# Kernel optimization log

Hardware: AMD Instinct MI355X
Metric: run time of the kernel (lower is better)

## Reference

```python
import jax, jax.numpy as jnp
import numpy as np

GROUPS = 32
EPS = 1e-5

def setup_inputs() -> dict:
    key = jax.random.key(0)
    k1, k2, k3 = jax.random.split(key, 3)
    C = 512
    x = jax.random.normal(k1, (4, C, 64, 64), dtype=jnp.float32)
    gn_weight = jnp.ones((C,), jnp.float32)
    gn_bias = jnp.zeros((C,), jnp.float32)
    qkv_weight = jax.random.normal(k2, (3 * C, C), jnp.float32) * (1.0 / np.sqrt(C))
    proj_weight = jax.random.normal(k3, (C, C), jnp.float32) * (1.0 / np.sqrt(C))
    proj_bias = jnp.zeros((C,), jnp.float32)
    return {"x": x, "gn_weight": gn_weight, "gn_bias": gn_bias,
            "qkv_weight": qkv_weight, "proj_weight": proj_weight, "proj_bias": proj_bias}

def reference(x, gn_weight, gn_bias, qkv_weight, proj_weight, proj_bias):
    n, c, h, w = x.shape
    residue = x
    # GroupNorm(32, c): normalize over (c//32 channels * h * w) per group
    xg = x.reshape(n, GROUPS, -1)
    mu = xg.mean(axis=-1, keepdims=True)
    var = xg.var(axis=-1, keepdims=True)
    xn = (xg - mu) * jax.lax.rsqrt(var + EPS)
    xn = xn.reshape(n, c, h, w) * gn_weight[None, :, None, None] + gn_bias[None, :, None, None]
    # tokens: [n, T, c] with T = h*w
    t = xn.reshape(n, c, h * w).transpose(0, 2, 1)
    # qkv linear (no bias), n_heads = 1 so head_size = c
    qkv = jnp.einsum('ntc,dc->ntd', t, qkv_weight)
    q, k, v = jnp.split(qkv, 3, axis=-1)
    scale = 1.0 / np.sqrt(c)
    scores = jnp.einsum('nqc,nkc->nqk', q, k) * scale  # [n, T, T]
    weights = jax.nn.softmax(scores, axis=-1)
    out = jnp.einsum('nqk,nkc->nqc', weights, v)
    out = jnp.einsum('ntc,dc->ntd', out, proj_weight) + proj_bias
    out = out.transpose(0, 2, 1).reshape(n, c, h, w)
    return out + residue
```

## Files before the change

### kernel.cpp

```cpp
#include <hip/hip_runtime.h>
#include <hip/hip_bf16.h>

typedef __bf16 bf16;
typedef __bf16 bf16x4 __attribute__((ext_vector_type(4)));
typedef __bf16 bf16x8 __attribute__((ext_vector_type(8)));
typedef float f32x4 __attribute__((ext_vector_type(4)));

__device__ __forceinline__ void gload_lds16(const bf16* g, bf16* l) {
    __builtin_amdgcn_global_load_lds(
        (const __attribute__((address_space(1))) void*)g,
        (__attribute__((address_space(3))) void*)l, 16, 0, 0);
}

__global__ __launch_bounds__(256) void k_pre(const float* __restrict__ x,
                                             const float* __restrict__ qw,
                                             const float* __restrict__ pw,
                                             float2* __restrict__ part,
                                             bf16* __restrict__ qwb,
                                             bf16* __restrict__ pwb) {
    const int b = blockIdx.x;
    if (b < 1024) {
        const float4* p = (const float4*)(x + (long)b * 8192);
        float s = 0.f, ss = 0.f;
        #pragma unroll
        for (int i = 0; i < 8; ++i) {
            float4 v = p[threadIdx.x + i * 256];
            s  += v.x + v.y + v.z + v.w;
            ss += v.x * v.x + v.y * v.y + v.z * v.z + v.w * v.w;
        }
        #pragma unroll
        for (int off = 32; off >= 1; off >>= 1) {
            s  += __shfl_down(s, off);
            ss += __shfl_down(ss, off);
        }
        __shared__ float rs[4], rss[4];
        if ((threadIdx.x & 63) == 0) { rs[threadIdx.x >> 6] = s; rss[threadIdx.x >> 6] = ss; }
        __syncthreads();
        if (threadIdx.x == 0)
            part[b] = make_float2(rs[0] + rs[1] + rs[2] + rs[3],
                                  rss[0] + rss[1] + rss[2] + rss[3]);
    } else {
        const int i = (b - 1024) * 256 + threadIdx.x;
        if (i < 786432) {
            float v = qw[i];
            if (i < 512 * 512) v *= 0.06376281516217733f;
            qwb[i] = (bf16)v;
        } else {
            const int j = i - 786432;
            pwb[j] = (bf16)pw[j];
        }
    }
}

__global__ __launch_bounds__(256) void k_norm_t(const float* __restrict__ x,
                                                const float* __restrict__ w,
                                                const float* __restrict__ b,
                                                const float2* __restrict__ part,
                                                bf16* __restrict__ t) {
    __shared__ float tile[64][65];
    __shared__ float2 sgs[4];
    const int bid = blockIdx.x;
    const int n = bid >> 9, rem = bid & 511;
    const int s0 = (rem >> 3) * 64, c0 = (rem & 7) * 64;
    const int tid = threadIdx.x;
    const int sl = tid & 63, cq = tid >> 6;
    if (tid < 4) {
        const float2* pp = part + ((long)(n * 32 + (c0 >> 4) + tid)) * 8;
        float S = 0.f, SS = 0.f;
        #pragma unroll
        for (int j = 0; j < 8; ++j) { S += pp[j].x; SS += pp[j].y; }
        const float mu = S * (1.f / 65536.f);
        const float var = SS * (1.f / 65536.f) - mu * mu;
        sgs[tid] = make_float2(mu, rsqrtf(var + 1e-5f));
    }
    __syncthreads();
    #pragma unroll
    for (int i = 0; i < 16; ++i) {
        const int cl = cq * 16 + i;
        const int c = c0 + cl;
        const float2 st = sgs[cl >> 4];
        const float v = x[((long)(n * 512 + c)) * 4096 + s0 + sl];
        tile[cl][sl] = (v - st.x) * st.y * w[c] + b[c];
    }
    __syncthreads();
    #pragma unroll
    for (int i = 0; i < 16; ++i) {
        const int sl2 = cq * 16 + i;
        const int cl2 = tid & 63;
        t[((long)(n * 4096 + s0 + sl2)) * 512 + c0 + cl2] = (bf16)tile[cl2][sl2];
    }
}

#define PH(mh, kk, S_, WN)                                                         \
  {                                                                                \
    if ((mh) == 0) {                                                               \
      _Pragma("unroll")                                                            \
      for (int n = 0; n < 4; ++n) {                                                \
        int row = wn * 64 + n * 16 + lr;                                           \
        int cg = lg ^ ((row >> 1) & 3);                                            \
        bfr[n] = *(const bf16x8*)(BsT + (kk) * 8192 + row * 32 + cg * 8);          \
      }                                                                            \
    }                                                                              \
    _Pragma("unroll")                                                              \
    for (int i = 0; i < 4; ++i) {                                                  \
      int row = wm * 128 + ((mh) * 4 + i) * 16 + lr;                               \
      int cg = lg ^ ((row >> 1) & 3);                                              \
      af[i] = *(const bf16x8*)(AsT + (kk) * 8192 + row * 32 + cg * 8);             \
    }                                                                              \
    if ((S_) >= 0) issue_unit(S_);                                                 \
    __builtin_amdgcn_s_barrier();                                                  \
    asm volatile("" ::: "memory");                                                 \
    __builtin_amdgcn_s_setprio(1);                                                 \
    _Pragma("unroll")                                                              \
    for (int i = 0; i < 4; ++i)                                                    \
      _Pragma("unroll")                                                            \
      for (int n = 0; n < 4; ++n)                                                  \
        acc[(mh) * 4 + i][n] =                                                     \
            __builtin_amdgcn_mfma_f32_16x16x32_bf16(af[i], bfr[n],                 \
                                                    acc[(mh) * 4 + i][n], 0, 0, 0);\
    __builtin_amdgcn_s_setprio(0);                                                 \
    if constexpr ((WN) >= 0)                                                       \
      asm volatile("s_waitcnt vmcnt(%0)" ::"i"(WN) : "memory");                    \
    __builtin_amdgcn_s_barrier();                                                  \
    asm volatile("" ::: "memory");                                                 \
  }

template <int EPI>
__global__ __launch_bounds__(512, 2) void gemm256(
    const bf16* __restrict__ A, int lda, long aZ,
    const bf16* __restrict__ B, int ldb, long bZ,
    bf16* __restrict__ C, int ldc, long cZ, int K,
    bf16* __restrict__ Vt) {
    __shared__ bf16 As[2 * 2 * 256 * 32];
    __shared__ bf16 Bs[2 * 2 * 256 * 32];
    const int t = threadIdx.x;
    const int wid = t >> 6, l = t & 63;
    const int wm = wid >> 2, wn = wid & 3;
    const int lr = l & 15;
    const int lg = l >> 4;
    const long z = blockIdx.z;

    const int gx = gridDim.x;
    int nwg = gx * gridDim.y;
    int flat = blockIdx.y * gx + blockIdx.x;
    if ((nwg & 7) == 0) { int qq = nwg >> 3; flat = (flat & 7) * qq + (flat >> 3); }
    const int bx = flat % gx, by = flat / gx;

    const bf16* Ab = A + z * aZ + (long)bx * 256 * lda;
    const bf16* Bb = B + z * bZ + (long)by * 256 * ldb;

    const int NT = K >> 6;
    const int NT4 = NT << 2;

    f32x4 acc[8][4];
    #pragma unroll
    for (int i = 0; i < 8; ++i)
        #pragma unroll
        for (int n = 0; n < 4; ++n) acc[i][n] = f32x4{0.f, 0.f, 0.f, 0.f};

    const int srow = t >> 2;
    const int scg0 = t & 3;

    auto issue_unit = [&](int s) {
        int ti = s >> 2, idx = s & 3;
        int kh = idx >> 1, isB = idx & 1;
        const bf16* g = isB ? Bb : Ab;
        int ld = isB ? ldb : lda;
        bf16* lp = (isB ? Bs : As) + ((ti & 1) * 2 + kh) * 8192;
        int k0 = ti * 64 + kh * 32;
        #pragma unroll
        for (int j = 0; j < 2; ++j) {
            int row = j * 128 + srow;
            int cg = scg0 ^ ((row >> 1) & 3);
            gload_lds16(g + (long)row * ld + k0 + cg * 8, lp + (j * 512 + t) * 8);
        }
    };

    #pragma unroll
    for (int s = 0; s < 6; ++s) issue_unit(s);
    asm volatile("s_waitcnt vmcnt(8)" ::: "memory");
    __builtin_amdgcn_s_barrier();
    asm volatile("" ::: "memory");

    bf16x8 bfr[4], af[4];

    for (int ti = 0; ti < NT - 2; ++ti) {
        const bf16* AsT = As + (ti & 1) * 16384;
        const bf16* BsT = Bs + (ti & 1) * 16384;
        const int sb = 4 * ti + 6;
        PH(0, 0, sb + 0, -1)
        PH(1, 0, sb + 1, 8)
        PH(0, 1, sb + 2, -1)
        PH(1, 1, sb + 3, 8)
    }
    {
        const bf16* AsT = As + ((NT - 2) & 1) * 16384;
        const bf16* BsT = Bs + ((NT - 2) & 1) * 16384;
        PH(0, 0, NT4 - 2, -1)
        PH(1, 0, NT4 - 1, 8)
        PH(0, 1, -1, -1)
        PH(1, 1, -1, 4)
    }
    {
        const bf16* AsT = As + ((NT - 1) & 1) * 16384;
        const bf16* BsT = Bs + ((NT - 1) & 1) * 16384;
        PH(0, 0, -1, -1)
        PH(1, 0, -1, 0)
        PH(0, 1, -1, -1)
        PH(1, 1, -1, -1)
    }

    const int row0 = bx * 256 + wm * 128;
    const int col0 = by * 256 + wn * 64;
    const int rq = lg * 4;

    if (EPI == 1) {
        bf16* Cz = C + z * cZ;
        #pragma unroll
        for (int i = 0; i < 8; ++i)
            #pragma unroll
            for (int n = 0; n < 4; ++n) {
                const int col = col0 + n * 16 + lr;
                #pragma unroll
                for (int r = 0; r < 4; ++r)
                    Cz[(long)(row0 + i * 16 + rq + r) * ldc + col] = (bf16)exp2f(acc[i][n][r]);
            }
    } else {
        if (by < 4) {
            #pragma unroll
            for (int i = 0; i < 8; ++i) {
                const int row = row0 + i * 16 + rq;
                #pragma unroll
                for (int n = 0; n < 4; ++n) {
                    const int col = col0 + n * 16 + lr;
                    #pragma unroll
                    for (int r = 0; r < 4; ++r)
                        C[(long)(row + r) * 1024 + col] = (bf16)acc[i][n][r];
                }
            }
        } else {
            const int d0 = by * 256 - 1024;
            const int rb0 = bx * 256;
            const int nb = rb0 >> 12;
            const int sp0 = rb0 & 4095;
            bf16* Lt = As;
            #pragma unroll 1
            for (int q = 0; q < 4; ++q) {
                if (wn == q) {
                    #pragma unroll
                    for (int n = 0; n < 4; ++n) {
                        const int dl = n * 16 + lr;
                        const int a = dl & 7;
                        #pragma unroll
                        for (int i = 0; i < 8; ++i) {
                            const int sp = wm * 128 + i * 16 + rq;
                            const int g = sp >> 3;
                            bf16x4 v;
                            v[0] = (bf16)acc[i][n][0]; v[1] = (bf16)acc[i][n][1];
                            v[2] = (bf16)acc[i][n][2]; v[3] = (bf16)acc[i][n][3];
                            *(bf16x4*)(Lt + dl * 264 + ((g ^ a) * 8) + (sp & 7)) = v;
                        }
                    }
                }
                __syncthreads();
                {
                    const int dl = t >> 3, c8 = t & 7, a2 = dl & 7;
                    bf16* vd = Vt + ((long)nb * 512 + d0 + q * 64 + dl) * 4096 + sp0;
                    #pragma unroll
                    for (int j = 0; j < 4; ++j) {
                        const int gr = c8 + j * 8;
                        bf16x8 vv = *(const bf16x8*)(Lt + dl * 264 + ((gr ^ a2) * 8));
                        *(bf16x8*)(vd + gr * 8) = vv;
                    }
                }
                __syncthreads();
            }
        }
    }
}

__global__ __launch_bounds__(512, 1) void k_pv(
    const bf16* __restrict__ P, const bf16* __restrict__ Vt,
    bf16* __restrict__ O, int ldo) {
    __shared__ bf16 Bs[2][512 * 64];
    __shared__ bf16 As[2][64 * 64];
    __shared__ float linv[64];
    const int t = threadIdx.x;
    const int w = t >> 6, l = t & 63, lr = l & 15, lg = l >> 4;
    const int lr7 = lr & 7;
    const int sr = t >> 3, sc8 = t & 7, sr7 = sr & 7;
    const long zz = blockIdx.y;
    const int bx = blockIdx.x;

    const bf16* Pg = P + zz * ((long)4096 * 4096) + (long)(bx * 64 + sr) * 4096 + (sc8 ^ sr7) * 8;
    const bf16* Vg = Vt + zz * ((long)512 * 4096) + (long)sr * 4096 + (sc8 ^ sr7) * 8;

    auto issue = [&](int tile, int buf) {
        gload_lds16(Pg + tile * 64, As[buf] + t * 8);
        #pragma unroll
        for (int u = 0; u < 8; ++u)
            gload_lds16(Vg + (long)u * 64 * 4096 + tile * 64, Bs[buf] + u * 4096 + t * 8);
    };

    f32x4 acc[4][4];
    #pragma unroll
    for (int i = 0; i < 4; ++i)
        #pragma unroll
        for (int n = 0; n < 4; ++n) acc[i][n] = f32x4{0.f, 0.f, 0.f, 0.f};

    float lsum = 0.f;

    issue(0, 0);
    issue(1, 1);

    for (int ti = 0; ti < 64; ++ti) {
        if (ti < 63) { asm volatile("s_waitcnt vmcnt(9)" ::: "memory"); }
        else         { asm volatile("s_waitcnt vmcnt(0)" ::: "memory"); }
        __builtin_amdgcn_s_barrier();
        asm volatile("" ::: "memory");

        const bf16* Asb = As[ti & 1];
        const bf16* Bsb = Bs[ti & 1];

        {
            bf16x8 sv = *(const bf16x8*)(Asb + t * 8);
            #pragma unroll
            for (int j = 0; j < 8; ++j) lsum += (float)sv[j];
        }

        __builtin_amdgcn_s_setprio(1);
        #pragma unroll
        for (int kk = 0; kk < 2; ++kk) {
            bf16x8 af[4], bfv[4];
            #pragma unroll
            for (int mi = 0; mi < 4; ++mi)
                af[mi] = *(const bf16x8*)(Asb + (mi * 16 + lr) * 64 + (((kk * 4 + lg) ^ lr7) * 8));
            #pragma unroll
            for (int n = 0; n < 4; ++n)
                bfv[n] = *(const bf16x8*)(Bsb + (w * 64 + n * 16 + lr) * 64 + (((kk * 4 + lg) ^ lr7) * 8));
            #pragma unroll
            for (int mi = 0; mi < 4; ++mi)
                #pragma unroll
                for (int n = 0; n < 4; ++n)
                    acc[mi][n] = __builtin_amdgcn_mfma_f32_16x16x32_bf16(af[mi], bfv[n], acc[mi][n], 0, 0, 0);
        }
        __builtin_amdgcn_s_setprio(0);

        __builtin_amdgcn_s_barrier();
        asm volatile("" ::: "memory");
        if (ti < 62) issue(ti + 2, ti & 1);
    }

    lsum += __shfl_xor(lsum, 1);
    lsum += __shfl_xor(lsum, 2);
    lsum += __shfl_xor(lsum, 4);
    if (sc8 == 0) linv[sr] = 1.f / lsum;
    asm volatile("s_waitcnt lgkmcnt(0)" ::: "memory");
    __builtin_amdgcn_s_barrier();
    asm volatile("" ::: "memory");

    bf16* Oz = O + zz * ((long)4096 * ldo);
    #pragma unroll
    for (int mi = 0; mi < 4; ++mi) {
        float4 lv = *(const float4*)&linv[mi * 16 + lg * 4];
        #pragma unroll
        for (int n = 0; n < 4; ++n) {
            const long base = (long)(bx * 64 + mi * 16 + lg * 4) * ldo + w * 64 + n * 16 + lr;
            Oz[base]           = (bf16)(acc[mi][n][0] * lv.x);
            Oz[base + ldo]     = (bf16)(acc[mi][n][1] * lv.y);
            Oz[base + 2 * ldo] = (bf16)(acc[mi][n][2] * lv.z);
            Oz[base + 3 * ldo] = (bf16)(acc[mi][n][3] * lv.w);
        }
    }
}

#define PH128(nh, kk, S_, WN)                                                      \
  {                                                                                \
    if ((nh) == 0) {                                                               \
      _Pragma("unroll")                                                            \
      for (int i = 0; i < 4; ++i) {                                                \
        int row = wm * 64 + i * 16 + lr;                                           \
        int cg = lg ^ ((row >> 1) & 3);                                            \
        af[i] = *(const bf16x8*)(AsT + (kk) * 8192 + row * 32 + cg * 8);           \
      }                                                                            \
    }                                                                              \
    _Pragma("unroll")                                                              \
    for (int j = 0; j < 2; ++j) {                                                  \
      int row = wn * 64 + ((nh) * 2 + j) * 16 + lr;                                \
      int cg = lg ^ ((row >> 1) & 3);                                              \
      bfr[j] = *(const bf16x8*)(BsT + (kk) * 4096 + row * 32 + cg * 8);            \
    }                                                                              \
    if ((S_) >= 0) issue_unit(S_);                                                 \
    __builtin_amdgcn_s_barrier();                                                  \
    asm volatile("" ::: "memory");                                                 \
    __builtin_amdgcn_s_setprio(1);                                                 \
    _Pragma("unroll")                                                              \
    for (int i = 0; i < 4; ++i)                                                    \
      _Pragma("unroll")                                                            \
      for (int j = 0; j < 2; ++j)                                                  \
        acc[i][(nh) * 2 + j] =                                                     \
            __builtin_amdgcn_mfma_f32_16x16x32_bf16(af[i], bfr[j],                 \
                                                    acc[i][(nh) * 2 + j], 0, 0, 0);\
    __builtin_amdgcn_s_setprio(0);                                                 \
    if constexpr ((WN) >= 0)                                                       \
      asm volatile("s_waitcnt vmcnt(%0)" ::"i"(WN) : "memory");                    \
    __builtin_amdgcn_s_barrier();                                                  \
    asm volatile("" ::: "memory");                                                 \
  }

__global__ __launch_bounds__(512, 2) void gemm_proj(
    const bf16* __restrict__ A, int lda,
    const bf16* __restrict__ B, int ldb,
    const float* __restrict__ bias,
    const float* __restrict__ xres,
    float* __restrict__ outp) {
    __shared__ bf16 As[2 * 2 * 256 * 32];
    __shared__ bf16 Bs[2 * 2 * 128 * 32];
    const int t = threadIdx.x;
    const int wid = t >> 6, l = t & 63;
    const int wm = wid >> 1, wn = wid & 1;
    const int lr = l & 15;
    const int lg = l >> 4;

    const int gx = gridDim.x;
    int nwg = gx * gridDim.y;
    int flat = blockIdx.y * gx + blockIdx.x;
    if ((nwg & 7) == 0) { int qq = nwg >> 3; flat = (flat & 7) * qq + (flat >> 3); }
    const int bx = flat % gx, by = flat / gx;

    const bf16* Ab = A + (long)bx * 256 * lda;
    const bf16* Bb = B + (long)by * 128 * ldb;

    const int NT = 8;
    const int NT4 = 32;

    f32x4 acc[4][4];
    #pragma unroll
    for (int i = 0; i < 4; ++i)
        #pragma unroll
        for (int n = 0; n < 4; ++n) acc[i][n] = f32x4{0.f, 0.f, 0.f, 0.f};

    const int srow = t >> 2;
    const int scg0 = t & 3;

    auto issue_unit = [&](int s) {
        int ti = s >> 2, idx = s & 3;
        int kh = idx >> 1, isB = idx & 1;
        int k0 = ti * 64 + kh * 32;
        if (isB) {
            bf16* lp = Bs + ((ti & 1) * 2 + kh) * 4096;
            int cg = scg0 ^ ((srow >> 1) & 3);
            gload_lds16(Bb + (long)srow * ldb + k0 + cg * 8, lp + t * 8);
        } else {
            bf16* lp = As + ((ti & 1) * 2 + kh) * 8192;
            #pragma unroll
            for (int j = 0; j < 2; ++j) {
                int row = j * 128 + srow;
                int cg = scg0 ^ ((row >> 1) & 3);
                gload_lds16(Ab + (long)row * lda + k0 + cg * 8, lp + (j * 512 + t) * 8);
            }
        }
    };

    #pragma unroll
    for (int s = 0; s < 6; ++s) issue_unit(s);
    asm volatile("s_waitcnt vmcnt(6)" ::: "memory");
    __builtin_amdgcn_s_barrier();
    asm volatile("" ::: "memory");

    bf16x8 bfr[2], af[4];

    for (int ti = 0; ti < NT - 2; ++ti) {
        const bf16* AsT = As + (ti & 1) * 16384;
        const bf16* BsT = Bs + (ti & 1) * 8192;
        const int sb = 4 * ti + 6;
        PH128(0, 0, sb + 0, -1)
        PH128(1, 0, sb + 1, 6)
        PH128(0, 1, sb + 2, -1)
        PH128(1, 1, sb + 3, 6)
    }
    {
        const bf16* AsT = As + ((NT - 2) & 1) * 16384;
        const bf16* BsT = Bs + ((NT - 2) & 1) * 8192;
        PH128(0, 0, NT4 - 2, -1)
        PH128(1, 0, NT4 - 1, 6)
        PH128(0, 1, -1, -1)
        PH128(1, 1, -1, 3)
    }
    {
        const bf16* AsT = As + ((NT - 1) & 1) * 16384;
        const bf16* BsT = Bs + ((NT - 1) & 1) * 8192;
        PH128(0, 0, -1, -1)
        PH128(1, 0, -1, 0)
        PH128(0, 1, -1, -1)
        PH128(1, 1, -1, -1)
    }

    const int r0 = bx * 256;
    const int c0b = by * 128;
    const int nb = r0 >> 12;
    const int sp0 = r0 & 4095;
    const int rq = lg * 4;
    float* Lt = (float*)As;
    #pragma unroll
    for (int q = 0; q < 4; ++q) {
        if (wn == (q >> 1)) {
            #pragma unroll
            for (int nn = 0; nn < 2; ++nn) {
                const int n = (q & 1) * 2 + nn;
                const int cl = nn * 16 + lr;
                #pragma unroll
                for (int i = 0; i < 4; ++i) {
                    const int sp = wm * 64 + i * 16 + rq;
                    float4 v;
                    v.x = acc[i][n][0]; v.y = acc[i][n][1];
                    v.z = acc[i][n][2]; v.w = acc[i][n][3];
                    *(float4*)(Lt + cl * 260 + sp) = v;
                }
            }
        }
        __syncthreads();
        {
            const int cl2 = t >> 4;
            const int spc = (t & 15) * 16;
            const int col = c0b + q * 32 + cl2;
            const float bb = bias[col];
            const long ob = ((long)nb * 512 + col) * 4096 + sp0 + spc;
            #pragma unroll
            for (int j = 0; j < 4; ++j) {
                float4 lv = *(const float4*)(Lt + cl2 * 260 + spc + j * 4);
                float4 xv = *(const float4*)(xres + ob + j * 4);
                float4 ov;
                ov.x = lv.x + bb + xv.x; ov.y = lv.y + bb + xv.y;
                ov.z = lv.z + bb + xv.z; ov.w = lv.w + bb + xv.w;
                *(float4*)(outp + ob + j * 4) = ov;
            }
        }
        __syncthreads();
    }
}

extern "C" void kernel_launch(void* const* d_in, const int* in_sizes, int n_in,
                              void* d_out, int out_size, void* d_ws, size_t ws_size,
                              hipStream_t stream) {
    const float* x     = (const float*)d_in[0];
    const float* gnw   = (const float*)d_in[1];
    const float* gnb   = (const float*)d_in[2];
    const float* qkvw  = (const float*)d_in[3];
    const float* projw = (const float*)d_in[4];
    const float* projb = (const float*)d_in[5];

    char* ws = (char*)d_ws;
    size_t off = 0;
    auto alloc = [&](size_t bytes) {
        void* p = ws + off;
        off += (bytes + 255) & ~(size_t)255;
        return p;
    };
    bf16*   qwb   = (bf16*)alloc((size_t)1536 * 512 * 2);
    bf16*   pwb   = (bf16*)alloc((size_t)512 * 512 * 2);
    float2* part  = (float2*)alloc((size_t)1024 * 8);
    bf16*   qk    = (bf16*)alloc((size_t)16384 * 1024 * 2);
    bf16*   Vt    = (bf16*)alloc((size_t)4 * 512 * 4096 * 2);
    char*   R     = (char*)alloc((size_t)4 * 4096 * 4096 * 2);
    bf16*   tbuf  = (bf16*)R;
    bf16*   Sbuf  = (bf16*)R;

    k_pre<<<5120, 256, 0, stream>>>(x, qkvw, projw, part, qwb, pwb);
    k_norm_t<<<2048, 256, 0, stream>>>(x, gnw, gnb, part, tbuf);

    gemm256<2><<<dim3(64, 6, 1), 512, 0, stream>>>(
        tbuf, 512, 0, qwb, 512, 0, qk, 1024, 0, 512, Vt);

    const long QZ = (long)4096 * 1024;
    const long SZ = (long)4096 * 4096;
    gemm256<1><<<dim3(16, 16, 4), 512, 0, stream>>>(
        qk, 1024, QZ,
        qk + 512, 1024, QZ,
        Sbuf, 4096, SZ, 512, nullptr);
    k_pv<<<dim3(64, 4), 512, 0, stream>>>(Sbuf, Vt, qk, 1024);

    gemm_proj<<<dim3(64, 4), 512, 0, stream>>>(
        qk, 1024, pwb, 512, projb, x, (float*)d_out);
}
```

Measured before the change: 288.8 us.

## Split PV kernel over head-dim halves with smaller blocks for more occupancy

```diff
diff --git a/kernel.cpp b/kernel.cpp
--- a/kernel.cpp
+++ b/kernel.cpp
@@ -279,27 +279,33 @@
     }
 }
 
-__global__ __launch_bounds__(512, 1) void k_pv(
+__global__ __launch_bounds__(256, 2) void k_pv(
     const bf16* __restrict__ P, const bf16* __restrict__ Vt,
     bf16* __restrict__ O, int ldo) {
-    __shared__ bf16 Bs[2][512 * 64];
+    __shared__ bf16 Bs[2][256 * 64];
     __shared__ bf16 As[2][64 * 64];
-    __shared__ float linv[64];
     const int t = threadIdx.x;
     const int w = t >> 6, l = t & 63, lr = l & 15, lg = l >> 4;
     const int lr7 = lr & 7;
-    const int sr = t >> 3, sc8 = t & 7, sr7 = sr & 7;
-    const long zz = blockIdx.y;
+    const int r8 = t >> 3, c8 = t & 7, s7 = r8 & 7;
+    const long zz = blockIdx.z;
+    const int dh = blockIdx.y;
     const int bx = blockIdx.x;
 
-    const bf16* Pg = P + zz * ((long)4096 * 4096) + (long)(bx * 64 + sr) * 4096 + (sc8 ^ sr7) * 8;
-    const bf16* Vg = Vt + zz * ((long)512 * 4096) + (long)sr * 4096 + (sc8 ^ sr7) * 8;
+    const bf16* Pg = P + zz * ((long)4096 * 4096)
+                       + (long)(bx * 64 + r8) * 4096 + (c8 ^ s7) * 8;
+    const bf16* Vg = Vt + zz * ((long)512 * 4096)
+                        + (long)(dh * 256 + r8) * 4096 + (c8 ^ s7) * 8;
 
     auto issue = [&](int tile, int buf) {
-        gload_lds16(Pg + tile * 64, As[buf] + t * 8);
+        #pragma unroll
+        for (int j = 0; j < 2; ++j)
+            gload_lds16(Pg + (long)j * 32 * 4096 + tile * 64,
+                        As[buf] + (j * 256 + t) * 8);
         #pragma unroll
         for (int u = 0; u < 8; ++u)
-            gload_lds16(Vg + (long)u * 64 * 4096 + tile * 64, Bs[buf] + u * 4096 + t * 8);
+            gload_lds16(Vg + (long)u * 32 * 4096 + tile * 64,
+                        Bs[buf] + (u * 256 + t) * 8);
     };
 
     f32x4 acc[4][4];
@@ -308,13 +314,13 @@
         #pragma unroll
         for (int n = 0; n < 4; ++n) acc[i][n] = f32x4{0.f, 0.f, 0.f, 0.f};
 
-    float lsum = 0.f;
+    float lsum0 = 0.f, lsum1 = 0.f;
 
     issue(0, 0);
     issue(1, 1);
 
     for (int ti = 0; ti < 64; ++ti) {
-        if (ti < 63) { asm volatile("s_waitcnt vmcnt(9)" ::: "memory"); }
+        if (ti < 63) { asm volatile("s_waitcnt vmcnt(10)" ::: "memory"); }
         else         { asm volatile("s_waitcnt vmcnt(0)" ::: "memory"); }
         __builtin_amdgcn_s_barrier();
         asm volatile("" ::: "memory");
@@ -323,9 +329,10 @@
         const bf16* Bsb = Bs[ti & 1];
 
         {
-            bf16x8 sv = *(const bf16x8*)(Asb + t * 8);
-            #pragma unroll
-            for (int j = 0; j < 8; ++j) lsum += (float)sv[j];
+            bf16x8 s0 = *(const bf16x8*)(Asb + t * 8);
+            bf16x8 s1 = *(const bf16x8*)(Asb + (256 + t) * 8);
+            #pragma unroll
+            for (int j = 0; j < 8; ++j) { lsum0 += (float)s0[j]; lsum1 += (float)s1[j]; }
         }
 
         __builtin_amdgcn_s_setprio(1);
@@ -351,10 +358,16 @@
         if (ti < 62) issue(ti + 2, ti & 1);
     }
 
-    lsum += __shfl_xor(lsum, 1);
-    lsum += __shfl_xor(lsum, 2);
-    lsum += __shfl_xor(lsum, 4);
-    if (sc8 == 0) linv[sr] = 1.f / lsum;
+    lsum0 += __shfl_xor(lsum0, 1);
+    lsum0 += __shfl_xor(lsum0, 2);
+    lsum0 += __shfl_xor(lsum0, 4);
+    lsum1 += __shfl_xor(lsum1, 1);
+    lsum1 += __shfl_xor(lsum1, 2);
+    lsum1 += __shfl_xor(lsum1, 4);
+    float* linv = (float*)&As[0][0];
+    __builtin_amdgcn_s_barrier();
+    asm volatile("" ::: "memory");
+    if (c8 == 0) { linv[r8] = 1.f / lsum0; linv[32 + r8] = 1.f / lsum1; }
     asm volatile("s_waitcnt lgkmcnt(0)" ::: "memory");
     __builtin_amdgcn_s_barrier();
     asm volatile("" ::: "memory");
@@ -365,7 +378,8 @@
         float4 lv = *(const float4*)&linv[mi * 16 + lg * 4];
         #pragma unroll
         for (int n = 0; n < 4; ++n) {
-            const long base = (long)(bx * 64 + mi * 16 + lg * 4) * ldo + w * 64 + n * 16 + lr;
+            const long base = (long)(bx * 64 + mi * 16 + lg * 4) * ldo
+                              + dh * 256 + w * 64 + n * 16 + lr;
             Oz[base]           = (bf16)(acc[mi][n][0] * lv.x);
             Oz[base + ldo]     = (bf16)(acc[mi][n][1] * lv.y);
             Oz[base + 2 * ldo] = (bf16)(acc[mi][n][2] * lv.z);
@@ -578,7 +592,7 @@
         qk, 1024, QZ,
         qk + 512, 1024, QZ,
         Sbuf, 4096, SZ, 512, nullptr);
-    k_pv<<<dim3(64, 4), 512, 0, stream>>>(Sbuf, Vt, qk, 1024);
+    k_pv<<<dim3(64, 2, 4), 256, 0, stream>>>(Sbuf, Vt, qk, 1024);
 
     gemm_proj<<<dim3(64, 4), 512, 0, stream>>>(
         qk, 1024, pwb, 512, projb, x, (float*)d_out);
```

Result: faster. 267.4 us (median of 2 runs) (-7.4%).
